# Performance work log

Measured on AMD Instinct MI355X. Metric: run time of the kernel, lower is better.

Reference implementation:

```python
import jax, jax.numpy as jnp
import numpy as np

N = 50000      # nodes
E = 800000     # edges (before self loops)
G = 64         # graphs in batch
IN = 128       # in_features
HID = 64       # hidden_dim per head
HEADS = 4
NC = 2         # num_classes
SLOPE = 0.2    # PyG GATConv negative_slope default


def setup_inputs() -> dict:
    key = jax.random.key(0)
    ks = jax.random.split(key, 16)
    s = 0.1
    HC = HID * HEADS
    inp = {
        "x": jax.random.normal(ks[0], (N, IN), jnp.float32),
        "edge_index": jax.random.randint(ks[1], (2, E), 0, N, jnp.int64),
        "batch": jnp.sort(jax.random.randint(ks[2], (N,), 0, G, jnp.int64)),
        # GATConv 1: lin weight [H*C, IN], att vecs [H, C], bias [H*C]
        "W1": jax.random.normal(ks[3], (HC, IN), jnp.float32) * s,
        "as1": jax.random.normal(ks[4], (HEADS, HID), jnp.float32) * s,
        "ad1": jax.random.normal(ks[5], (HEADS, HID), jnp.float32) * s,
        "b1": jnp.zeros((HC,), jnp.float32),
        # GATConv 2
        "W2": jax.random.normal(ks[6], (HC, HC), jnp.float32) * s,
        "as2": jax.random.normal(ks[7], (HEADS, HID), jnp.float32) * s,
        "ad2": jax.random.normal(ks[8], (HEADS, HID), jnp.float32) * s,
        "b2": jnp.zeros((HC,), jnp.float32),
        # GATConv 3
        "W3": jax.random.normal(ks[9], (HC, HC), jnp.float32) * s,
        "as3": jax.random.normal(ks[10], (HEADS, HID), jnp.float32) * s,
        "ad3": jax.random.normal(ks[11], (HEADS, HID), jnp.float32) * s,
        "b3": jnp.zeros((HC,), jnp.float32),
        # MLP head
        "fc1_w": jax.random.normal(ks[12], (HID, HC), jnp.float32) * s,
        "fc1_b": jnp.zeros((HID,), jnp.float32),
        "fc2_w": jax.random.normal(ks[13], (NC, HID), jnp.float32) * s,
        "fc2_b": jnp.zeros((NC,), jnp.float32),
    }
    return inp


def gat_conv(x, src, dst, W, a_src, a_dst, b):
    """PyG-style GATConv (concat=True, self loops already in src/dst)."""
    n = x.shape[0]
    h = (x @ W.T).reshape(n, HEADS, HID)            # [N,H,C]
    al_s = jnp.sum(h * a_src[None], axis=-1)        # [N,H]
    al_d = jnp.sum(h * a_dst[None], axis=-1)        # [N,H]
    e = jax.nn.leaky_relu(al_s[src] + al_d[dst], SLOPE)  # [Et,H]
    # segment softmax over edges grouped by destination node
    m = jax.ops.segment_max(e, dst, num_segments=n)      # [N,H]
    ex = jnp.exp(e - m[dst])
    den = jax.ops.segment_sum(ex, dst, num_segments=n)
    alpha = ex / (den[dst] + 1e-16)                      # [Et,H]
    out = jax.ops.segment_sum(h[src] * alpha[:, :, None], dst, num_segments=n)
    return out.reshape(n, HEADS * HID) + b


def reference(x, edge_index, batch, W1, as1, ad1, b1, W2, as2, ad2, b2,
              W3, as3, ad3, b3, fc1_w, fc1_b, fc2_w, fc2_b):
    loops = jnp.arange(N, dtype=edge_index.dtype)
    src = jnp.concatenate([edge_index[0], loops])   # add_self_loops=True
    dst = jnp.concatenate([edge_index[1], loops])

    h = jax.nn.relu(gat_conv(x, src, dst, W1, as1, ad1, b1))
    h = jax.nn.relu(gat_conv(h, src, dst, W2, as2, ad2, b2))
    h = gat_conv(h, src, dst, W3, as3, ad3, b3)

    # global_mean_pool over batch vector
    sums = jax.ops.segment_sum(h, batch, num_segments=G)          # [G,H*C]
    cnts = jax.ops.segment_sum(jnp.ones((N,), h.dtype), batch, num_segments=G)
    pooled = sums / jnp.maximum(cnts, 1.0)[:, None]

    z = jax.nn.relu(pooled @ fc1_w.T + fc1_b)
    return z @ fc2_w.T + fc2_b                                    # [G,NC]
```

## Files before the change

### kernel.cpp

```cpp
#include <hip/hip_runtime.h>
#include <hip/hip_bf16.h>

#define N_NODES 50000
#define E_EDGES 800000
#define ET (E_EDGES + N_NODES)
#define G_GRAPHS 64
#define IN_F 128
#define HID 64
#define HEADS 4
#define HC (HID * HEADS)
#define NC 2
#define SLOPE 0.2f
#define L2E 1.4426950408889634f

typedef float f32x4 __attribute__((ext_vector_type(4)));
typedef __bf16 bf16x8 __attribute__((ext_vector_type(8)));
typedef unsigned short us8 __attribute__((ext_vector_type(8)));
typedef unsigned short us4 __attribute__((ext_vector_type(4)));
typedef _Float16 h16x4 __attribute__((ext_vector_type(4)));

#define MFMA16(a, b, c) \
  __builtin_amdgcn_mfma_f32_16x16x32_bf16(__builtin_bit_cast(bf16x8, (a)), \
                                          __builtin_bit_cast(bf16x8, (b)), (c), 0, 0, 0)

__device__ inline unsigned short f2bf_rne(float f) {
  unsigned u = __builtin_bit_cast(unsigned, f);
  u += 0x7fffu + ((u >> 16) & 1u);
  return (unsigned short)(u >> 16);
}
__device__ inline float bf2f(unsigned short h) {
  unsigned u = ((unsigned)h) << 16;
  return __builtin_bit_cast(float, u);
}


__device__ inline void split4(const float* __restrict__ in, unsigned short* __restrict__ hi,
                              unsigned short* __restrict__ lo, int i) {
  float4 v = *(const float4*)&in[i];
  float f[4] = {v.x, v.y, v.z, v.w};
  us4 h, l;
#pragma unroll
  for (int j = 0; j < 4; j++) {
    unsigned short hb = f2bf_rne(f[j]);
    h[j] = hb;
    l[j] = f2bf_rne(f[j] - bf2f(hb));
  }
  *(us4*)&hi[i] = h;
  *(us4*)&lo[i] = l;
}

#define QX (N_NODES * IN_F / 4)
#define QW1 (HC * IN_F / 4)
#define QW2 (HC * HC / 4)
#define QTOT (QX + QW1 + 2 * QW2)

__global__ __launch_bounds__(256) void split_all_kernel(
    const float* __restrict__ x, const float* __restrict__ W1,
    const float* __restrict__ W2, const float* __restrict__ W3,
    unsigned short* __restrict__ xhi,
    unsigned short* __restrict__ w1h, unsigned short* __restrict__ w1l,
    unsigned short* __restrict__ w2h, unsigned short* __restrict__ w2l,
    unsigned short* __restrict__ w3h, unsigned short* __restrict__ w3l) {
  int q = blockIdx.x * 256 + threadIdx.x;
  if (q < QX) {
    int i = q * 4;
    float4 v = *(const float4*)&x[i];
    float f[4] = {v.x, v.y, v.z, v.w};
    us4 h;
#pragma unroll
    for (int j = 0; j < 4; j++) h[j] = f2bf_rne(f[j]);
    *(us4*)&xhi[i] = h;
  } else if (q < QX + QW1) {
    split4(W1, w1h, w1l, (q - QX) * 4);
  } else if (q < QX + QW1 + QW2) {
    split4(W2, w2h, w2l, (q - QX - QW1) * 4);
  } else {
    split4(W3, w3h, w3l, (q - QX - QW1 - QW2) * 4);
  }
}


__global__ void count_kernel(const int* __restrict__ ei, int* __restrict__ cnt) {
  int e = blockIdx.x * blockDim.x + threadIdx.x;
  if (e >= ET) return;
  int dst = (e < E_EDGES) ? ei[E_EDGES + e] : (e - E_EDGES);
  atomicAdd(&cnt[dst], 1);
}

#define SCAN_BLOCKS ((N_NODES + 255) / 256)

__global__ __launch_bounds__(256) void scan1_kernel(const int* __restrict__ cnt,
                                                    int* __restrict__ incl_buf,
                                                    int* __restrict__ partial) {
  __shared__ int ws[4];
  int tid = threadIdx.x, b = blockIdx.x;
  int wave = tid >> 6, lane = tid & 63;
  int i = b * 256 + tid;
  int v = (i < N_NODES) ? cnt[i] : 0;
  int x = v;
#pragma unroll
  for (int off = 1; off < 64; off <<= 1) {
    int t = __shfl_up(x, off, 64);
    if (lane >= off) x += t;
  }
  if (lane == 63) ws[wave] = x;
  __syncthreads();
  if (tid == 0) {
    int s = 0;
#pragma unroll
    for (int w = 0; w < 4; w++) { int t = ws[w]; ws[w] = s; s += t; }
    partial[b] = s;
  }
  __syncthreads();
  if (i < N_NODES) incl_buf[i] = x + ws[wave];
}

__global__ __launch_bounds__(256) void scan2_kernel(int* __restrict__ partial) {
  __shared__ int ws[4];
  int tid = threadIdx.x;
  int wave = tid >> 6, lane = tid & 63;
  int v = (tid < SCAN_BLOCKS) ? partial[tid] : 0;
  int x = v;
#pragma unroll
  for (int off = 1; off < 64; off <<= 1) {
    int t = __shfl_up(x, off, 64);
    if (lane >= off) x += t;
  }
  if (lane == 63) ws[wave] = x;
  __syncthreads();
  if (tid == 0) {
    int s = 0;
#pragma unroll
    for (int w = 0; w < 4; w++) { int t = ws[w]; ws[w] = s; s += t; }
  }
  __syncthreads();
  partial[tid] = x + ws[wave] - v;
}

__global__ __launch_bounds__(256) void scan3_kernel(const int* __restrict__ cnt,
                                                    int* __restrict__ incl_buf,
                                                    const int* __restrict__ partial,
                                                    int* __restrict__ rowptr,
                                                    int* __restrict__ cursor) {
  int tid = threadIdx.x, b = blockIdx.x;
  int i = b * 256 + tid;
  if (i >= N_NODES) return;
  int incl = incl_buf[i] + partial[b];
  rowptr[i + 1] = incl;
  cursor[i] = incl - cnt[i];
  if (i == 0) rowptr[0] = 0;
}

__global__ void scatter_kernel(const int* __restrict__ ei, int* __restrict__ cursor,
                               int* __restrict__ csr_src) {
  int e = blockIdx.x * blockDim.x + threadIdx.x;
  if (e >= ET) return;
  int src, dst;
  if (e < E_EDGES) { src = ei[e]; dst = ei[E_EDGES + e]; }
  else { src = e - E_EDGES; dst = src; }
  int pos = atomicAdd(&cursor[dst], 1);
  csr_src[pos] = src;
}


template <int K>
__global__ __launch_bounds__(256) void mfma_gemm_kernel(
    const unsigned short* __restrict__ A,
    const unsigned short* __restrict__ Whi, const unsigned short* __restrict__ Wlo,
    const float* __restrict__ a_s, const float* __restrict__ a_d,
    _Float16* __restrict__ hbuf16, float* __restrict__ als, float* __restrict__ ald) {
  __shared__ unsigned short As[4 * 128 * 8];
  __shared__ unsigned short Bs[2][4 * 256 * 8];

  int t = threadIdx.x;
  int mt = blockIdx.x;
  int w = t >> 6, lane = t & 63, lr = lane & 15, kg = lane >> 4;
  int srow = t >> 2, skg = t & 3;

  f32x4 acc[8][4];
#pragma unroll
  for (int m = 0; m < 8; m++)
#pragma unroll
    for (int nf = 0; nf < 4; nf++) {
      f32x4 z = {0.f, 0.f, 0.f, 0.f};
      acc[m][nf] = z;
    }

  for (int k0 = 0; k0 < K; k0 += 32) {
    us8 va[2];
#pragma unroll
    for (int i = 0; i < 2; i++) {
      int agrow = mt * 128 + srow + 64 * i;
      if (agrow < N_NODES) {
        va[i] = *(const us8*)&A[(size_t)agrow * K + k0 + skg * 8];
      } else {
        us8 z = {0, 0, 0, 0, 0, 0, 0, 0};
        va[i] = z;
      }
    }
    us8 vb0[4], vb1[4];
#pragma unroll
    for (int c = 0; c < 4; c++) {
      int n = srow + 64 * c;
      vb0[c] = *(const us8*)&Whi[(size_t)n * K + k0 + skg * 8];
      vb1[c] = *(const us8*)&Wlo[(size_t)n * K + k0 + skg * 8];
    }
    __syncthreads();
#pragma unroll
    for (int i = 0; i < 2; i++) {
      int row = srow + 64 * i;
      *(us8*)&As[(skg * 128 + row) * 8] = va[i];
    }
#pragma unroll
    for (int c = 0; c < 4; c++) {
      int n = srow + 64 * c;
      *(us8*)&Bs[0][(skg * 256 + n) * 8] = vb0[c];
      *(us8*)&Bs[1][(skg * 256 + n) * 8] = vb1[c];
    }
    __syncthreads();

    us8 bh[4], bl[4];
#pragma unroll
    for (int nf = 0; nf < 4; nf++) {
      int n = w * 64 + nf * 16 + lr;
      bh[nf] = *(us8*)&Bs[0][(kg * 256 + n) * 8];
      bl[nf] = *(us8*)&Bs[1][(kg * 256 + n) * 8];
    }
#pragma unroll
    for (int m = 0; m < 8; m++) {
      int row = m * 16 + lr;
      us8 ah = *(us8*)&As[(kg * 128 + row) * 8];
#pragma unroll
      for (int nf = 0; nf < 4; nf++) {
        acc[m][nf] = MFMA16(ah, bh[nf], acc[m][nf]);
        acc[m][nf] = MFMA16(ah, bl[nf], acc[m][nf]);
      }
    }
  }

  int head = w;
  float asv[4], adv[4];
#pragma unroll
  for (int nf = 0; nf < 4; nf++) {
    asv[nf] = a_s[head * HID + nf * 16 + lr];
    adv[nf] = a_d[head * HID + nf * 16 + lr];
  }
#pragma unroll
  for (int m = 0; m < 8; m++) {
#pragma unroll
    for (int r = 0; r < 4; r++) {
      int grow = mt * 128 + m * 16 + kg * 4 + r;
      float ps = 0.f, pd = 0.f;
#pragma unroll
      for (int nf = 0; nf < 4; nf++) {
        float v = acc[m][nf][r];
        ps += v * asv[nf];
        pd += v * adv[nf];
        if (grow < N_NODES)
          hbuf16[(size_t)grow * HC + head * 64 + nf * 16 + lr] = (_Float16)v;
      }
#pragma unroll
      for (int msk = 1; msk < 16; msk <<= 1) {
        ps += __shfl_xor(ps, msk, 64);
        pd += __shfl_xor(pd, msk, 64);
      }
      if (lr == 0 && grow < N_NODES) {
        als[grow * HEADS + head] = ps * L2E;
        ald[grow * HEADS + head] = pd * L2E;
      }
    }
  }
}


template <int MODE>
__global__ __launch_bounds__(256) void agg_kernel(
    const _Float16* __restrict__ hbuf16, const float* __restrict__ alsE,
    const float* __restrict__ aldE, const int* __restrict__ rowptr,
    const int* __restrict__ csr_src, const float* __restrict__ bias,
    unsigned short* __restrict__ ohi, float* __restrict__ pooled,
    const int* __restrict__ batch) {
  int wave = threadIdx.x >> 6;
  int lane = threadIdx.x & 63;
  int v = blockIdx.x * 4 + wave;
  int head = lane >> 4;
  float myald = aldE[(unsigned)v * HEADS + head];
  int beg = rowptr[v], end = rowptr[v + 1];

  float den = 0.f;
  f32x4 acc = {0.f, 0.f, 0.f, 0.f};
  const _Float16* hp = hbuf16 + (lane << 2);
#pragma unroll 4
  for (int i = beg; i < end; i++) {
    int s = csr_src[i];
    float a = alsE[(unsigned)s * HEADS + head] + myald;
    a = fmaxf(a, SLOPE * a);
    float ex = __builtin_amdgcn_exp2f(a);
    den += ex;
    h16x4 hv = *(const h16x4*)(hp + ((unsigned)s << 8));
    acc[0] += (float)hv[0] * ex;
    acc[1] += (float)hv[1] * ex;
    acc[2] += (float)hv[2] * ex;
    acc[3] += (float)hv[3] * ex;
  }
  float inv = 1.0f / (den + 1e-16f);
  float4 bv = *(const float4*)&bias[lane * 4];
  float o[4];
  o[0] = acc[0] * inv + bv.x;
  o[1] = acc[1] * inv + bv.y;
  o[2] = acc[2] * inv + bv.z;
  o[3] = acc[3] * inv + bv.w;

  if (MODE == 0) {
    us4 h;
#pragma unroll
    for (int j = 0; j < 4; j++) {
      o[j] = fmaxf(o[j], 0.f);
      h[j] = f2bf_rne(o[j]);
    }
    *(us4*)&ohi[(size_t)v * HC + lane * 4] = h;
  } else {
    __shared__ float pacc[4][HC];
    __shared__ int pg[4];
    f32x4 ov = {o[0], o[1], o[2], o[3]};
    *(f32x4*)&pacc[wave][lane * 4] = ov;
    if (lane == 0) pg[wave] = batch[v];
    __syncthreads();
    int c = threadIdx.x;
    int g0 = pg[0], g1 = pg[1], g2 = pg[2], g3 = pg[3];
    if (g0 == g1 && g1 == g2 && g2 == g3) {
      atomicAdd(&pooled[g0 * HC + c], pacc[0][c] + pacc[1][c] + pacc[2][c] + pacc[3][c]);
    } else {
      atomicAdd(&pooled[g0 * HC + c], pacc[0][c]);
      atomicAdd(&pooled[g1 * HC + c], pacc[1][c]);
      atomicAdd(&pooled[g2 * HC + c], pacc[2][c]);
      atomicAdd(&pooled[g3 * HC + c], pacc[3][c]);
    }
  }
}


__global__ __launch_bounds__(64) void mlp_kernel(const float* __restrict__ pooled_sum,
                                                 const int* __restrict__ batch,
                                                 const float* __restrict__ w1,
                                                 const float* __restrict__ b1,
                                                 const float* __restrict__ w2,
                                                 const float* __restrict__ b2,
                                                 float* __restrict__ out) {
  int g = blockIdx.x;
  int j = threadIdx.x;
  int lo = 0, hi = N_NODES;
  while (lo < hi) { int mid = (lo + hi) >> 1; if (batch[mid] < g) lo = mid + 1; else hi = mid; }
  int start = lo;
  hi = N_NODES;
  while (lo < hi) { int mid = (lo + hi) >> 1; if (batch[mid] < g + 1) lo = mid + 1; else hi = mid; }
  float invc = 1.0f / fmaxf((float)(lo - start), 1.0f);
  __shared__ float z[HID];
  float acc = 0.f;
  for (int k = 0; k < HC; k++) acc += pooled_sum[g * HC + k] * w1[j * HC + k];
  z[j] = fmaxf(acc * invc + b1[j], 0.f);
  __syncthreads();
  if (j < NC) {
    float o = b2[j];
    for (int k = 0; k < HID; k++) o += z[k] * w2[j * HID + k];
    out[g * NC + j] = o;
  }
}


extern "C" void kernel_launch(void* const* d_in, const int* in_sizes, int n_in,
                              void* d_out, int out_size, void* d_ws, size_t ws_size,
                              hipStream_t stream) {
  const float* x    = (const float*)d_in[0];
  const int*   ei   = (const int*)d_in[1];
  const int*   batch= (const int*)d_in[2];
  const float* W1   = (const float*)d_in[3];
  const float* as1  = (const float*)d_in[4];
  const float* ad1  = (const float*)d_in[5];
  const float* b1   = (const float*)d_in[6];
  const float* W2   = (const float*)d_in[7];
  const float* as2  = (const float*)d_in[8];
  const float* ad2  = (const float*)d_in[9];
  const float* b2   = (const float*)d_in[10];
  const float* W3   = (const float*)d_in[11];
  const float* as3  = (const float*)d_in[12];
  const float* ad3  = (const float*)d_in[13];
  const float* b3   = (const float*)d_in[14];
  const float* fc1w = (const float*)d_in[15];
  const float* fc1b = (const float*)d_in[16];
  const float* fc2w = (const float*)d_in[17];
  const float* fc2b = (const float*)d_in[18];
  float* out = (float*)d_out;

  char* ws = (char*)d_ws;
  size_t off = 0;
  _Float16* hbuf16 = (_Float16*)(ws + off); off += (size_t)N_NODES * HC * 2;
  unsigned short* ahi = (unsigned short*)(ws + off); off += (size_t)N_NODES * HC * 2;
  unsigned short* xhi = (unsigned short*)(ws + off); off += (size_t)N_NODES * IN_F * 2;
  unsigned short* w1h = (unsigned short*)(ws + off); off += (size_t)HC * IN_F * 2;
  unsigned short* w1l = (unsigned short*)(ws + off); off += (size_t)HC * IN_F * 2;
  unsigned short* w2h = (unsigned short*)(ws + off); off += (size_t)HC * HC * 2;
  unsigned short* w2l = (unsigned short*)(ws + off); off += (size_t)HC * HC * 2;
  unsigned short* w3h = (unsigned short*)(ws + off); off += (size_t)HC * HC * 2;
  unsigned short* w3l = (unsigned short*)(ws + off); off += (size_t)HC * HC * 2;
  float* als    = (float*)(ws + off); off += (size_t)N_NODES * HEADS * 4;
  float* ald    = (float*)(ws + off); off += (size_t)N_NODES * HEADS * 4;
  float* pooled = (float*)(ws + off); off += (size_t)G_GRAPHS * HC * 4;
  int*   cnt    = (int*)(ws + off);   off += (size_t)N_NODES * 4;
  int*   cursor = (int*)(ws + off);   off += (size_t)N_NODES * 4;
  int*   csrsrc = (int*)(ws + off);   off += (size_t)ET * 4;
  int*   rowptr = (int*)(ws + off);   off += (size_t)(N_NODES + 1) * 4;
  int*   partial= (int*)(ws + off);   off += 256 * 4;

  split_all_kernel<<<(QTOT + 255) / 256, 256, 0, stream>>>(
      x, W1, W2, W3, xhi, w1h, w1l, w2h, w2l, w3h, w3l);

  hipMemsetAsync(cnt, 0, (size_t)N_NODES * 4, stream);
  hipMemsetAsync(pooled, 0, (size_t)G_GRAPHS * HC * 4, stream);
  count_kernel<<<(ET + 255) / 256, 256, 0, stream>>>(ei, cnt);
  scan1_kernel<<<SCAN_BLOCKS, 256, 0, stream>>>(cnt, cursor, partial);
  scan2_kernel<<<1, 256, 0, stream>>>(partial);
  scan3_kernel<<<SCAN_BLOCKS, 256, 0, stream>>>(cnt, cursor, partial, rowptr, cursor);
  scatter_kernel<<<(ET + 255) / 256, 256, 0, stream>>>(ei, cursor, csrsrc);

  dim3 gemm_grid((N_NODES + 127) / 128);
  int agg_grid = N_NODES / 4;

  mfma_gemm_kernel<IN_F><<<gemm_grid, 256, 0, stream>>>(xhi, w1h, w1l, as1, ad1, hbuf16, als, ald);
  agg_kernel<0><<<agg_grid, 256, 0, stream>>>(hbuf16, als, ald, rowptr, csrsrc, b1, ahi, nullptr, nullptr);
  mfma_gemm_kernel<HC><<<gemm_grid, 256, 0, stream>>>(ahi, w2h, w2l, as2, ad2, hbuf16, als, ald);
  agg_kernel<0><<<agg_grid, 256, 0, stream>>>(hbuf16, als, ald, rowptr, csrsrc, b2, ahi, nullptr, nullptr);
  mfma_gemm_kernel<HC><<<gemm_grid, 256, 0, stream>>>(ahi, w3h, w3l, as3, ad3, hbuf16, als, ald);
  agg_kernel<1><<<agg_grid, 256, 0, stream>>>(hbuf16, als, ald, rowptr, csrsrc, b3, nullptr, pooled, batch);

  mlp_kernel<<<G_GRAPHS, 64, 0, stream>>>(pooled, batch, fc1w, fc1b, fc2w, fc2b, out);
}
```

Before: 460.5 us.

## Shrink GEMM row tile to 64 and process two nodes per wave in aggregation

The GEMM tile drops from 128 to 64 rows per block, which doubles the block count and halves the accumulator registers, aiming at higher occupancy and better load balance across CUs. The aggregation kernel now has each wave handle two destination nodes with interleaved edge loops, so two independent gather chains are in flight per iteration to hide memory latency. The shorter node's loads are clamped to its last edge and masked out, which wastes some work when degrees differ. Pooling now merges runs of equal graph ids across the eight nodes in a block to issue fewer atomics.

```diff
diff --git a/kernel.cpp b/kernel.cpp
--- a/kernel.cpp
+++ b/kernel.cpp
@@ -169,7 +169,7 @@
     const unsigned short* __restrict__ Whi, const unsigned short* __restrict__ Wlo,
     const float* __restrict__ a_s, const float* __restrict__ a_d,
     _Float16* __restrict__ hbuf16, float* __restrict__ als, float* __restrict__ ald) {
-  __shared__ unsigned short As[4 * 128 * 8];
+  __shared__ unsigned short As[4 * 64 * 8];
   __shared__ unsigned short Bs[2][4 * 256 * 8];
 
   int t = threadIdx.x;
@@ -177,26 +177,25 @@
   int w = t >> 6, lane = t & 63, lr = lane & 15, kg = lane >> 4;
   int srow = t >> 2, skg = t & 3;
 
-  f32x4 acc[8][4];
-#pragma unroll
-  for (int m = 0; m < 8; m++)
+  f32x4 acc[4][4];
+#pragma unroll
+  for (int m = 0; m < 4; m++)
 #pragma unroll
     for (int nf = 0; nf < 4; nf++) {
       f32x4 z = {0.f, 0.f, 0.f, 0.f};
       acc[m][nf] = z;
     }
 
+  int agrow = mt * 64 + srow;
+  bool avalid = agrow < N_NODES;
+
   for (int k0 = 0; k0 < K; k0 += 32) {
-    us8 va[2];
-#pragma unroll
-    for (int i = 0; i < 2; i++) {
-      int agrow = mt * 128 + srow + 64 * i;
-      if (agrow < N_NODES) {
-        va[i] = *(const us8*)&A[(size_t)agrow * K + k0 + skg * 8];
-      } else {
-        us8 z = {0, 0, 0, 0, 0, 0, 0, 0};
-        va[i] = z;
-      }
+    us8 va;
+    if (avalid) {
+      va = *(const us8*)&A[(size_t)agrow * K + k0 + skg * 8];
+    } else {
+      us8 z = {0, 0, 0, 0, 0, 0, 0, 0};
+      va = z;
     }
     us8 vb0[4], vb1[4];
 #pragma unroll
@@ -206,11 +205,7 @@
       vb1[c] = *(const us8*)&Wlo[(size_t)n * K + k0 + skg * 8];
     }
     __syncthreads();
-#pragma unroll
-    for (int i = 0; i < 2; i++) {
-      int row = srow + 64 * i;
-      *(us8*)&As[(skg * 128 + row) * 8] = va[i];
-    }
+    *(us8*)&As[(skg * 64 + srow) * 8] = va;
 #pragma unroll
     for (int c = 0; c < 4; c++) {
       int n = srow + 64 * c;
@@ -227,9 +222,9 @@
       bl[nf] = *(us8*)&Bs[1][(kg * 256 + n) * 8];
     }
 #pragma unroll
-    for (int m = 0; m < 8; m++) {
+    for (int m = 0; m < 4; m++) {
       int row = m * 16 + lr;
-      us8 ah = *(us8*)&As[(kg * 128 + row) * 8];
+      us8 ah = *(us8*)&As[(kg * 64 + row) * 8];
 #pragma unroll
       for (int nf = 0; nf < 4; nf++) {
         acc[m][nf] = MFMA16(ah, bh[nf], acc[m][nf]);
@@ -246,10 +241,10 @@
     adv[nf] = a_d[head * HID + nf * 16 + lr];
   }
 #pragma unroll
-  for (int m = 0; m < 8; m++) {
+  for (int m = 0; m < 4; m++) {
 #pragma unroll
     for (int r = 0; r < 4; r++) {
-      int grow = mt * 128 + m * 16 + kg * 4 + r;
+      int grow = mt * 64 + m * 16 + kg * 4 + r;
       float ps = 0.f, pd = 0.f;
 #pragma unroll
       for (int nf = 0; nf < 4; nf++) {
@@ -282,60 +277,80 @@
     const int* __restrict__ batch) {
   int wave = threadIdx.x >> 6;
   int lane = threadIdx.x & 63;
-  int v = blockIdx.x * 4 + wave;
+  int v0 = blockIdx.x * 8 + wave * 2;
+  int v1 = v0 + 1;
   int head = lane >> 4;
-  float myald = aldE[(unsigned)v * HEADS + head];
-  int beg = rowptr[v], end = rowptr[v + 1];
-
-  float den = 0.f;
-  f32x4 acc = {0.f, 0.f, 0.f, 0.f};
+  float ald0 = aldE[(unsigned)v0 * HEADS + head];
+  float ald1 = aldE[(unsigned)v1 * HEADS + head];
+  int beg0 = rowptr[v0], n0 = rowptr[v0 + 1] - beg0;
+  int beg1 = rowptr[v1], n1 = rowptr[v1 + 1] - beg1;
+  int n = max(n0, n1);
+
+  float den0 = 0.f, den1 = 0.f;
+  f32x4 acc0 = {0.f, 0.f, 0.f, 0.f};
+  f32x4 acc1 = {0.f, 0.f, 0.f, 0.f};
   const _Float16* hp = hbuf16 + (lane << 2);
-#pragma unroll 4
-  for (int i = beg; i < end; i++) {
-    int s = csr_src[i];
-    float a = alsE[(unsigned)s * HEADS + head] + myald;
-    a = fmaxf(a, SLOPE * a);
-    float ex = __builtin_amdgcn_exp2f(a);
-    den += ex;
-    h16x4 hv = *(const h16x4*)(hp + ((unsigned)s << 8));
-    acc[0] += (float)hv[0] * ex;
-    acc[1] += (float)hv[1] * ex;
-    acc[2] += (float)hv[2] * ex;
-    acc[3] += (float)hv[3] * ex;
-  }
-  float inv = 1.0f / (den + 1e-16f);
+#pragma unroll 2
+  for (int i = 0; i < n; i++) {
+    int s0 = csr_src[beg0 + min(i, n0 - 1)];
+    int s1 = csr_src[beg1 + min(i, n1 - 1)];
+    float a0 = alsE[(unsigned)s0 * HEADS + head] + ald0;
+    float a1 = alsE[(unsigned)s1 * HEADS + head] + ald1;
+    a0 = fmaxf(a0, SLOPE * a0);
+    a1 = fmaxf(a1, SLOPE * a1);
+    float ex0 = (i < n0) ? __builtin_amdgcn_exp2f(a0) : 0.f;
+    float ex1 = (i < n1) ? __builtin_amdgcn_exp2f(a1) : 0.f;
+    h16x4 h0 = *(const h16x4*)(hp + ((unsigned)s0 << 8));
+    h16x4 h1 = *(const h16x4*)(hp + ((unsigned)s1 << 8));
+    den0 += ex0; den1 += ex1;
+    acc0[0] += (float)h0[0] * ex0; acc0[1] += (float)h0[1] * ex0;
+    acc0[2] += (float)h0[2] * ex0; acc0[3] += (float)h0[3] * ex0;
+    acc1[0] += (float)h1[0] * ex1; acc1[1] += (float)h1[1] * ex1;
+    acc1[2] += (float)h1[2] * ex1; acc1[3] += (float)h1[3] * ex1;
+  }
+  float inv0 = 1.0f / (den0 + 1e-16f);
+  float inv1 = 1.0f / (den1 + 1e-16f);
   float4 bv = *(const float4*)&bias[lane * 4];
-  float o[4];
-  o[0] = acc[0] * inv + bv.x;
-  o[1] = acc[1] * inv + bv.y;
-  o[2] = acc[2] * inv + bv.z;
-  o[3] = acc[3] * inv + bv.w;
+  float o0[4], o1[4];
+  o0[0] = acc0[0] * inv0 + bv.x; o0[1] = acc0[1] * inv0 + bv.y;
+  o0[2] = acc0[2] * inv0 + bv.z; o0[3] = acc0[3] * inv0 + bv.w;
+  o1[0] = acc1[0] * inv1 + bv.x; o1[1] = acc1[1] * inv1 + bv.y;
+  o1[2] = acc1[2] * inv1 + bv.z; o1[3] = acc1[3] * inv1 + bv.w;
 
   if (MODE == 0) {
-    us4 h;
+    us4 h0, h1;
 #pragma unroll
     for (int j = 0; j < 4; j++) {
-      o[j] = fmaxf(o[j], 0.f);
-      h[j] = f2bf_rne(o[j]);
-    }
-    *(us4*)&ohi[(size_t)v * HC + lane * 4] = h;
+      h0[j] = f2bf_rne(fmaxf(o0[j], 0.f));
+      h1[j] = f2bf_rne(fmaxf(o1[j], 0.f));
+    }
+    *(us4*)&ohi[(size_t)v0 * HC + lane * 4] = h0;
+    *(us4*)&ohi[(size_t)v1 * HC + lane * 4] = h1;
   } else {
-    __shared__ float pacc[4][HC];
-    __shared__ int pg[4];
-    f32x4 ov = {o[0], o[1], o[2], o[3]};
-    *(f32x4*)&pacc[wave][lane * 4] = ov;
-    if (lane == 0) pg[wave] = batch[v];
+    __shared__ float pacc[8][HC];
+    __shared__ int pg[8];
+    f32x4 ov0 = {o0[0], o0[1], o0[2], o0[3]};
+    f32x4 ov1 = {o1[0], o1[1], o1[2], o1[3]};
+    *(f32x4*)&pacc[wave * 2][lane * 4] = ov0;
+    *(f32x4*)&pacc[wave * 2 + 1][lane * 4] = ov1;
+    if (lane == 0) {
+      pg[wave * 2] = batch[v0];
+      pg[wave * 2 + 1] = batch[v1];
+    }
     __syncthreads();
     int c = threadIdx.x;
-    int g0 = pg[0], g1 = pg[1], g2 = pg[2], g3 = pg[3];
-    if (g0 == g1 && g1 == g2 && g2 == g3) {
-      atomicAdd(&pooled[g0 * HC + c], pacc[0][c] + pacc[1][c] + pacc[2][c] + pacc[3][c]);
-    } else {
-      atomicAdd(&pooled[g0 * HC + c], pacc[0][c]);
-      atomicAdd(&pooled[g1 * HC + c], pacc[1][c]);
-      atomicAdd(&pooled[g2 * HC + c], pacc[2][c]);
-      atomicAdd(&pooled[g3 * HC + c], pacc[3][c]);
-    }
+    float s = pacc[0][c];
+    int gcur = pg[0];
+#pragma unroll
+    for (int wv = 1; wv < 8; wv++) {
+      if (pg[wv] != gcur) {
+        atomicAdd(&pooled[gcur * HC + c], s);
+        s = 0.f;
+        gcur = pg[wv];
+      }
+      s += pacc[wv][c];
+    }
+    atomicAdd(&pooled[gcur * HC + c], s);
   }
 }
 
@@ -423,8 +438,8 @@
   scan3_kernel<<<SCAN_BLOCKS, 256, 0, stream>>>(cnt, cursor, partial, rowptr, cursor);
   scatter_kernel<<<(ET + 255) / 256, 256, 0, stream>>>(ei, cursor, csrsrc);
 
-  dim3 gemm_grid((N_NODES + 127) / 128);
-  int agg_grid = N_NODES / 4;
+  dim3 gemm_grid((N_NODES + 63) / 64);
+  int agg_grid = N_NODES / 8;
 
   mfma_gemm_kernel<IN_F><<<gemm_grid, 256, 0, stream>>>(xhi, w1h, w1l, as1, ad1, hbuf16, als, ald);
   agg_kernel<0><<<agg_grid, 256, 0, stream>>>(hbuf16, als, ald, rowptr, csrsrc, b1, ahi, nullptr, nullptr);
```

After: 428.3 us. 7.0% less time.

## Batch edge attention across lanes in aggregation and halve GEMM row tile

Applied to the files above, without the earlier changes.

The aggregation kernel now loads 16 neighbor indices at once (one per lane within each head group), computes their attention exponents in parallel, then broadcasts index and weight to all lanes via ds_bpermute for the feature gather. This removes the serial per-edge dependent index load and exp from the inner loop, at the cost of a cross-lane reduction of the denominator and extra permute instructions. Separately, the GEMM tile drops from 128 to 64 rows per block, doubling the grid for better CU occupancy, but each block still loads the full weight tile, so more weight loads are needed per output row.

```diff
diff --git a/kernel.cpp b/kernel.cpp
--- a/kernel.cpp
+++ b/kernel.cpp
@@ -169,7 +169,7 @@
     const unsigned short* __restrict__ Whi, const unsigned short* __restrict__ Wlo,
     const float* __restrict__ a_s, const float* __restrict__ a_d,
     _Float16* __restrict__ hbuf16, float* __restrict__ als, float* __restrict__ ald) {
-  __shared__ unsigned short As[4 * 128 * 8];
+  __shared__ unsigned short As[4 * 64 * 8];
   __shared__ unsigned short Bs[2][4 * 256 * 8];
 
   int t = threadIdx.x;
@@ -177,26 +177,25 @@
   int w = t >> 6, lane = t & 63, lr = lane & 15, kg = lane >> 4;
   int srow = t >> 2, skg = t & 3;
 
-  f32x4 acc[8][4];
-#pragma unroll
-  for (int m = 0; m < 8; m++)
+  f32x4 acc[4][4];
+#pragma unroll
+  for (int m = 0; m < 4; m++)
 #pragma unroll
     for (int nf = 0; nf < 4; nf++) {
       f32x4 z = {0.f, 0.f, 0.f, 0.f};
       acc[m][nf] = z;
     }
 
+  int agrow = mt * 64 + srow;
+  bool avalid = agrow < N_NODES;
+
   for (int k0 = 0; k0 < K; k0 += 32) {
-    us8 va[2];
-#pragma unroll
-    for (int i = 0; i < 2; i++) {
-      int agrow = mt * 128 + srow + 64 * i;
-      if (agrow < N_NODES) {
-        va[i] = *(const us8*)&A[(size_t)agrow * K + k0 + skg * 8];
-      } else {
-        us8 z = {0, 0, 0, 0, 0, 0, 0, 0};
-        va[i] = z;
-      }
+    us8 va;
+    if (avalid) {
+      va = *(const us8*)&A[(size_t)agrow * K + k0 + skg * 8];
+    } else {
+      us8 z = {0, 0, 0, 0, 0, 0, 0, 0};
+      va = z;
     }
     us8 vb0[4], vb1[4];
 #pragma unroll
@@ -206,11 +205,7 @@
       vb1[c] = *(const us8*)&Wlo[(size_t)n * K + k0 + skg * 8];
     }
     __syncthreads();
-#pragma unroll
-    for (int i = 0; i < 2; i++) {
-      int row = srow + 64 * i;
-      *(us8*)&As[(skg * 128 + row) * 8] = va[i];
-    }
+    *(us8*)&As[(skg * 64 + srow) * 8] = va;
 #pragma unroll
     for (int c = 0; c < 4; c++) {
       int n = srow + 64 * c;
@@ -227,9 +222,9 @@
       bl[nf] = *(us8*)&Bs[1][(kg * 256 + n) * 8];
     }
 #pragma unroll
-    for (int m = 0; m < 8; m++) {
+    for (int m = 0; m < 4; m++) {
       int row = m * 16 + lr;
-      us8 ah = *(us8*)&As[(kg * 128 + row) * 8];
+      us8 ah = *(us8*)&As[(kg * 64 + row) * 8];
 #pragma unroll
       for (int nf = 0; nf < 4; nf++) {
         acc[m][nf] = MFMA16(ah, bh[nf], acc[m][nf]);
@@ -246,10 +241,10 @@
     adv[nf] = a_d[head * HID + nf * 16 + lr];
   }
 #pragma unroll
-  for (int m = 0; m < 8; m++) {
+  for (int m = 0; m < 4; m++) {
 #pragma unroll
     for (int r = 0; r < 4; r++) {
-      int grow = mt * 128 + m * 16 + kg * 4 + r;
+      int grow = mt * 64 + m * 16 + kg * 4 + r;
       float ps = 0.f, pd = 0.f;
 #pragma unroll
       for (int nf = 0; nf < 4; nf++) {
@@ -284,25 +279,56 @@
   int lane = threadIdx.x & 63;
   int v = blockIdx.x * 4 + wave;
   int head = lane >> 4;
+  int lr = lane & 15;
   float myald = aldE[(unsigned)v * HEADS + head];
-  int beg = rowptr[v], end = rowptr[v + 1];
+  int beg = rowptr[v];
+  int n = rowptr[v + 1] - beg;
 
   float den = 0.f;
   f32x4 acc = {0.f, 0.f, 0.f, 0.f};
   const _Float16* hp = hbuf16 + (lane << 2);
-#pragma unroll 4
-  for (int i = beg; i < end; i++) {
-    int s = csr_src[i];
+  int bpbase = (lane & 48) << 2;
+
+  for (int c = 0; c < n; c += 16) {
+    int e = c + lr;
+    int s = csr_src[beg + min(e, n - 1)];
     float a = alsE[(unsigned)s * HEADS + head] + myald;
     a = fmaxf(a, SLOPE * a);
-    float ex = __builtin_amdgcn_exp2f(a);
+    float ex = (e < n) ? __builtin_amdgcn_exp2f(a) : 0.f;
     den += ex;
-    h16x4 hv = *(const h16x4*)(hp + ((unsigned)s << 8));
-    acc[0] += (float)hv[0] * ex;
-    acc[1] += (float)hv[1] * ex;
-    acc[2] += (float)hv[2] * ex;
-    acc[3] += (float)hv[3] * ex;
-  }
+    int rem = n - c;
+    if (rem >= 16) {
+#pragma unroll
+      for (int j = 0; j < 16; j++) {
+        int bp = bpbase + (j << 2);
+        int sj = __builtin_amdgcn_ds_bpermute(bp, s);
+        float exj = __builtin_bit_cast(
+            float, __builtin_amdgcn_ds_bpermute(bp, __builtin_bit_cast(int, ex)));
+        h16x4 hv = *(const h16x4*)(hp + ((unsigned)sj << 8));
+        acc[0] += (float)hv[0] * exj;
+        acc[1] += (float)hv[1] * exj;
+        acc[2] += (float)hv[2] * exj;
+        acc[3] += (float)hv[3] * exj;
+      }
+    } else {
+      for (int j = 0; j < rem; j++) {
+        int bp = bpbase + (j << 2);
+        int sj = __builtin_amdgcn_ds_bpermute(bp, s);
+        float exj = __builtin_bit_cast(
+            float, __builtin_amdgcn_ds_bpermute(bp, __builtin_bit_cast(int, ex)));
+        h16x4 hv = *(const h16x4*)(hp + ((unsigned)sj << 8));
+        acc[0] += (float)hv[0] * exj;
+        acc[1] += (float)hv[1] * exj;
+        acc[2] += (float)hv[2] * exj;
+        acc[3] += (float)hv[3] * exj;
+      }
+    }
+  }
+  den += __shfl_xor(den, 1, 64);
+  den += __shfl_xor(den, 2, 64);
+  den += __shfl_xor(den, 4, 64);
+  den += __shfl_xor(den, 8, 64);
+
   float inv = 1.0f / (den + 1e-16f);
   float4 bv = *(const float4*)&bias[lane * 4];
   float o[4];
@@ -314,10 +340,7 @@
   if (MODE == 0) {
     us4 h;
 #pragma unroll
-    for (int j = 0; j < 4; j++) {
-      o[j] = fmaxf(o[j], 0.f);
-      h[j] = f2bf_rne(o[j]);
-    }
+    for (int j = 0; j < 4; j++) h[j] = f2bf_rne(fmaxf(o[j], 0.f));
     *(us4*)&ohi[(size_t)v * HC + lane * 4] = h;
   } else {
     __shared__ float pacc[4][HC];
@@ -326,15 +349,15 @@
     *(f32x4*)&pacc[wave][lane * 4] = ov;
     if (lane == 0) pg[wave] = batch[v];
     __syncthreads();
-    int c = threadIdx.x;
+    int c2 = threadIdx.x;
     int g0 = pg[0], g1 = pg[1], g2 = pg[2], g3 = pg[3];
     if (g0 == g1 && g1 == g2 && g2 == g3) {
-      atomicAdd(&pooled[g0 * HC + c], pacc[0][c] + pacc[1][c] + pacc[2][c] + pacc[3][c]);
+      atomicAdd(&pooled[g0 * HC + c2], pacc[0][c2] + pacc[1][c2] + pacc[2][c2] + pacc[3][c2]);
     } else {
-      atomicAdd(&pooled[g0 * HC + c], pacc[0][c]);
-      atomicAdd(&pooled[g1 * HC + c], pacc[1][c]);
-      atomicAdd(&pooled[g2 * HC + c], pacc[2][c]);
-      atomicAdd(&pooled[g3 * HC + c], pacc[3][c]);
+      atomicAdd(&pooled[g0 * HC + c2], pacc[0][c2]);
+      atomicAdd(&pooled[g1 * HC + c2], pacc[1][c2]);
+      atomicAdd(&pooled[g2 * HC + c2], pacc[2][c2]);
+      atomicAdd(&pooled[g3 * HC + c2], pacc[3][c2]);
     }
   }
 }
@@ -423,7 +446,7 @@
   scan3_kernel<<<SCAN_BLOCKS, 256, 0, stream>>>(cnt, cursor, partial, rowptr, cursor);
   scatter_kernel<<<(ET + 255) / 256, 256, 0, stream>>>(ei, cursor, csrsrc);
 
-  dim3 gemm_grid((N_NODES + 127) / 128);
+  dim3 gemm_grid((N_NODES + 63) / 64);
   int agg_grid = N_NODES / 4;
 
   mfma_gemm_kernel<IN_F><<<gemm_grid, 256, 0, stream>>>(xhi, w1h, w1l, as1, ad1, hbuf16, als, ald);
```

Result: no change. 458.5 us (-0.4%).
